# Kernel tuning notes

Measured on AMD Instinct MI355X. Metric: run time of the kernel, lower is better.

The kernel has to match this reference:

```python
import jax, jax.numpy as jnp
import numpy as np

B = 1
H_IMG, W_IMG = 64, 64
NF = H_IMG * W_IMG          # 4096 front/query tokens
NS = 1024                   # satellite tokens (32x32 grid)
SAT_IN, FRONT_IN = 768, 320
NH, HD = 8, 64
MD = NH * HD                # 512
GHID, GHD = 128, 16
GMD = NH * GHD              # 128
GEO_RATIO, ROPE_BASE = 0.5, 10000.0
LAMBDA_GEO, LAMBDA_GEOM = 1.0, 1.0
EPS = 1e-5


def _linear(x, w, b):
    return x @ w.T + b


def _layernorm(x, g, b):
    m = x.mean(-1, keepdims=True)
    v = jnp.var(x, axis=-1, keepdims=True)
    return (x - m) / jnp.sqrt(v + EPS) * g + b


def _georope(t, xy):
    """Continuous 2D (x,y) rotary embedding on the first GEO_RATIO fraction of head_dim.
    t: [B,NH,N,HD], xy: [B,N,2]."""
    rot = int(HD * GEO_RATIO)       # rotated dims (32)
    axis = rot // 2                 # dims per spatial axis (16)
    half = axis // 2                # frequency pairs per axis (8)
    inv_freq = ROPE_BASE ** (-jnp.arange(half, dtype=t.dtype) / half)

    def rot_axis(a, coord):
        th = coord[:, None, :, None] * inv_freq   # [B,1,N,half]
        c, s = jnp.cos(th), jnp.sin(th)
        a1, a2 = a[..., :half], a[..., half:]
        return jnp.concatenate([a1 * c - a2 * s, a1 * s + a2 * c], axis=-1)

    tx = rot_axis(t[..., :axis], xy[..., 0])
    ty = rot_axis(t[..., axis:rot], xy[..., 1])
    return jnp.concatenate([tx, ty, t[..., rot:]], axis=-1)


def _heads(x, hd):
    b, n, _ = x.shape
    return x.reshape(b, n, NH, hd).transpose(0, 2, 1, 3)


def setup_inputs() -> dict:
    key = jax.random.key(0)
    ks = iter(jax.random.split(key, 64))

    def w(*shape):
        return jax.random.normal(next(ks), shape, jnp.float32) / np.sqrt(shape[-1]).astype(np.float32)

    z = lambda n: jnp.zeros((n,), jnp.float32)
    o = lambda n: jnp.ones((n,), jnp.float32)
    return {
        "front_feat": jax.random.normal(next(ks), (B, FRONT_IN, H_IMG, W_IMG), jnp.float32),
        "front_bev_xy": jax.random.uniform(next(ks), (B, NF, 2), jnp.float32, -1.0, 1.0),
        "sat_tokens": jax.random.normal(next(ks), (B, NS, SAT_IN), jnp.float32),
        "sat_xy": jax.random.uniform(next(ks), (B, NS, 2), jnp.float32, -1.0, 1.0),
        "front_plucker": jax.random.normal(next(ks), (B, NF, 6), jnp.float32),
        "pos_w1": w(MD, 2), "pos_b1": z(MD), "pos_w2": w(MD, MD), "pos_b2": z(MD),
        "fa_w": w(MD, FRONT_IN), "fa_b": z(MD), "fa_ln_g": o(MD), "fa_ln_b": z(MD),
        "qn_g": o(MD), "qn_b": z(MD),
        "sa_w": w(MD, SAT_IN), "sa_b": z(MD), "sa_ln_g": o(MD), "sa_ln_b": z(MD),
        "wq": w(MD, MD), "bq": z(MD), "wk": w(MD, MD), "bk": z(MD), "wv": w(MD, MD), "bv": z(MD),
        "plk_w1": w(GHID, 6), "plk_b1": z(GHID), "plk_w2": w(GHID, GHID), "plk_b2": z(GHID),
        "sxy_w1": w(GHID, 2), "sxy_b1": z(GHID), "sxy_w2": w(GHID, GHID), "sxy_b2": z(GHID),
        "gqn_g": o(GHID), "gqn_b": z(GHID), "gkn_g": o(GHID), "gkn_b": z(GHID),
        "wqg": w(GMD, GHID), "bqg": z(GMD), "wkg": w(GMD, GHID), "bkg": z(GMD),
    }


def reference(front_feat, front_bev_xy, sat_tokens, sat_xy, front_plucker,
              pos_w1, pos_b1, pos_w2, pos_b2, fa_w, fa_b, fa_ln_g, fa_ln_b,
              qn_g, qn_b, sa_w, sa_b, sa_ln_g, sa_ln_b, wq, bq, wk, bk, wv, bv,
              plk_w1, plk_b1, plk_w2, plk_b2, sxy_w1, sxy_b1, sxy_w2, sxy_b2,
              gqn_g, gqn_b, gkn_g, gkn_b, wqg, bqg, wkg, bkg):
    b = front_feat.shape[0]
    ff = front_feat.reshape(b, FRONT_IN, NF).transpose(0, 2, 1)      # [B,NF,C]
    pos = _linear(jax.nn.silu(_linear(front_bev_xy, pos_w1, pos_b1)), pos_w2, pos_b2)
    feat = _layernorm(_linear(ff, fa_w, fa_b), fa_ln_g, fa_ln_b)
    q_embed = _layernorm(pos + feat, qn_g, qn_b)
    sat_feat = _layernorm(_linear(sat_tokens, sa_w, sa_b), sa_ln_g, sa_ln_b)
    q = _heads(_linear(q_embed, wq, bq), HD)                         # [B,H,NF,HD]
    k = _heads(_linear(sat_feat, wk, bk), HD)                        # [B,H,NS,HD]
    v = _heads(_linear(sat_feat, wv, bv), HD)
    qr = _georope(q, front_bev_xy)
    kr = _georope(k, sat_xy)
    logits = jnp.einsum('bhqd,bhkd->bhqk', qr, kr) / np.float32(np.sqrt(HD))
    # learned geometric Q/K stream (Plucker rays vs sat xy)
    plk = _layernorm(_linear(jax.nn.silu(_linear(front_plucker, plk_w1, plk_b1)), plk_w2, plk_b2), gqn_g, gqn_b)
    sgf = _layernorm(_linear(jax.nn.silu(_linear(sat_xy, sxy_w1, sxy_b1)), sxy_w2, sxy_b2), gkn_g, gkn_b)
    qg = _heads(_linear(plk, wqg, bqg), GHD)
    kg = _heads(_linear(sgf, wkg, bkg), GHD)
    logits = logits + LAMBDA_GEOM * (jnp.einsum('bhqd,bhkd->bhqk', qg, kg) / np.float32(np.sqrt(GHD)))
    # additive pairwise squared-distance bias, broadcast over heads
    dist2 = ((front_bev_xy[:, :, None, :] - sat_xy[:, None, :, :]) ** 2).sum(-1)   # [B,NF,NS]
    logits = logits - LAMBDA_GEO * dist2[:, None]
    attn = jax.nn.softmax(logits, axis=-1)
    read = jnp.einsum('bhqk,bhkd->bhqd', attn, v)
    return read.transpose(0, 2, 1, 3).reshape(b, NF, MD)
```

## Files before the change

kernel.cpp:

```cpp
#include <hip/hip_runtime.h>
#include <hip/hip_bf16.h>
#include <stdint.h>

#define NF 4096
#define NS 1024
#define MD 512
#define HD 64
#define DA 96
#define GHID 128

#define L2E 1.44269504f
#define S2L 1.6986436f
#define SMAX 12.0f

typedef unsigned short u16;
typedef __attribute__((ext_vector_type(8))) short bf8v;
typedef __attribute__((ext_vector_type(4))) float f4v;

__device__ __forceinline__ u16 f2bf(float f) {
  __hip_bfloat16 h = __float2bfloat16(f);
  return __builtin_bit_cast(u16, h);
}
__device__ __forceinline__ float bf2f(u16 u) {
  union { unsigned u; float f; } v; v.u = ((unsigned)u) << 16; return v.f;
}
__device__ __forceinline__ f4v mfma16(bf8v a, bf8v b, f4v c) {
  return __builtin_amdgcn_mfma_f32_16x16x32_bf16(a, b, c, 0, 0, 0);
}
__device__ __forceinline__ void gld16(const void* g, void* l) {
  __builtin_amdgcn_global_load_lds(
      (const __attribute__((address_space(1))) unsigned int*)g,
      (__attribute__((address_space(3))) unsigned int*)l, 16, 0, 0);
}

#define OFF_POSW2 0
#define OFF_FAW   262144
#define OFF_SAW   425984
#define OFF_WQ    819200
#define OFF_WKV   1081344
#define OFF_PLKW2 1605632
#define OFF_SXYW2 1622016
#define OFF_WQG   1638400
#define OFF_WKG   1654784
#define OFF_SATT  1671168
#define TOTW      2457600

#define EPI_OUT  0
#define EPI_ROPE 1
#define EPI_VT   2
#define EPI_GEO  3

__global__ __launch_bounds__(256) void k_l0(
    const float* __restrict__ s0, const float* __restrict__ s1,
    const float* __restrict__ s2, const float* __restrict__ s3,
    const float* __restrict__ s4, const float* __restrict__ s5,
    const float* __restrict__ s6, const float* __restrict__ s7,
    const float* __restrict__ s8, const float* __restrict__ s9,
    const float* __restrict__ s10, u16* __restrict__ pool,
    const float* __restrict__ bk, const float* __restrict__ bv,
    float* __restrict__ bkv,
    const float* __restrict__ ff, u16* __restrict__ ffT,
    const float* __restrict__ in0, const float* __restrict__ w0,
    const float* __restrict__ b0, u16* __restrict__ o0,
    const float* __restrict__ in1, const float* __restrict__ w1,
    const float* __restrict__ b1, u16* __restrict__ o1,
    const float* __restrict__ in2, const float* __restrict__ w2,
    const float* __restrict__ b2, u16* __restrict__ o2,
    u16* __restrict__ Qaug, u16* __restrict__ Kaug, float* __restrict__ kk2) {
  __shared__ u16 sT[32][72];
  int blk = blockIdx.x, t = threadIdx.x;
  if (blk < 2401) {
    int i4 = blk * 256 + t;
    if (i4 < TOTW / 4) {
      int idx = i4 * 4;
      const float* src; int off;
      if      (idx < OFF_FAW)   { src = s0;  off = OFF_POSW2; }
      else if (idx < OFF_SAW)   { src = s1;  off = OFF_FAW; }
      else if (idx < OFF_WQ)    { src = s2;  off = OFF_SAW; }
      else if (idx < OFF_WKV)   { src = s3;  off = OFF_WQ; }
      else if (idx < 1343488)   { src = s4;  off = OFF_WKV; }
      else if (idx < OFF_PLKW2) { src = s5;  off = 1343488; }
      else if (idx < OFF_SXYW2) { src = s6;  off = OFF_PLKW2; }
      else if (idx < OFF_WQG)   { src = s7;  off = OFF_SXYW2; }
      else if (idx < OFF_WKG)   { src = s8;  off = OFF_WQG; }
      else if (idx < OFF_SATT)  { src = s9;  off = OFF_WKG; }
      else                      { src = s10; off = OFF_SATT; }
      float4 v = *(const float4*)(src + (idx - off));
      ushort4 o;
      o.x = f2bf(v.x); o.y = f2bf(v.y); o.z = f2bf(v.z); o.w = f2bf(v.w);
      *(ushort4*)(pool + idx) = o;
    } else if (i4 < TOTW / 4 + 256) {
      int j = (i4 - TOTW / 4) * 4;
#pragma unroll
      for (int e = 0; e < 4; ++e) {
        int b = j + e;
        bkv[b] = (b < 512) ? bk[b] : bv[b - 512];
      }
    }
  } else if (blk < 3041) {
    int lb = blk - 2401;
    int n0 = (lb & 63) * 64, c0 = (lb >> 6) * 32;
    {
      int cr = t >> 3, nc = (t & 7) * 8;
      const float* src = ff + (size_t)(c0 + cr) * NF + n0 + nc;
      float4 v0 = *(const float4*)src, v1 = *(const float4*)(src + 4);
      bf8v p;
      p[0]=(short)f2bf(v0.x); p[1]=(short)f2bf(v0.y); p[2]=(short)f2bf(v0.z); p[3]=(short)f2bf(v0.w);
      p[4]=(short)f2bf(v1.x); p[5]=(short)f2bf(v1.y); p[6]=(short)f2bf(v1.z); p[7]=(short)f2bf(v1.w);
      *(bf8v*)&sT[cr][nc] = p;
    }
    __syncthreads();
    {
      int r = t >> 2, cc = (t & 3) * 8;
      bf8v p;
#pragma unroll
      for (int e = 0; e < 8; ++e) p[e] = (short)sT[cc + e][r];
      *(bf8v*)(ffT + (size_t)(n0 + r) * 320 + c0 + cc) = p;
    }
  } else if (blk < 13793) {
    int lb = blk - 3041;
    const float *in, *w, *b; u16* o; int mlog, K, idx;
    if (lb < 8192)       { in = in0; w = w0; b = b0; o = o0; mlog = 9; K = 2; idx = lb * 256 + t; }
    else if (lb < 10240) { in = in1; w = w1; b = b1; o = o1; mlog = 7; K = 6; idx = (lb - 8192) * 256 + t; }
    else                 { in = in2; w = w2; b = b2; o = o2; mlog = 7; K = 2; idx = (lb - 10240) * 256 + t; }
    int M = 1 << mlog;
    int n = idx >> mlog, m = idx & (M - 1);
    float acc = b[m];
    for (int k = 0; k < K; ++k) acc += in[n * K + k] * w[m * K + k];
    o[idx] = f2bf(acc / (1.f + __expf(-acc)));
  } else {
    int id = (blk - 13793) * 256 + t;
    int side = id >= NF * 8;
    int lid = side ? id - NF * 8 : id;
    int n = lid >> 3, h = lid & 7;
    const float* xy = side ? in2 : in0;
    u16* aug = side ? Kaug : Qaug;
    int nrows = side ? NS : NF;
    float x = xy[n * 2], y = xy[n * 2 + 1];
    bf8v p0, z;
#pragma unroll
    for (int e = 0; e < 8; ++e) { p0[e] = 0; z[e] = 0; }
    p0[0] = (short)f2bf(S2L * x);
    p0[1] = (short)f2bf(S2L * y);
    u16* dst = aug + ((size_t)h * nrows + n) * DA + 80;
    *(bf8v*)dst = p0;
    *(bf8v*)(dst + 8) = z;
    if (side && h == 0) kk2[n] = L2E * (x * x + y * y) + SMAX;
  }
}

__device__ __forceinline__ void gemm_body(const u16* __restrict__ A, const u16* __restrict__ W,
                                          const float* __restrict__ bias, u16* __restrict__ out,
                                          int m0, int n0, int N, int K,
                                          int mode, float scale, const float* __restrict__ xy,
                                          u16* __restrict__ aug, int nrows) {
  constexpr int MR = 2, NR = 2;
  __shared__ u16 sA[2][64 * 64];
  __shared__ u16 sB[2][64 * 64];
  const int tid = threadIdx.x, w = tid >> 6, lane = tid & 63;
  const int l16 = lane & 15, lh = lane >> 4;
  const int wr = w >> 1, wc = w & 1;

  f4v acc[MR][NR];
#pragma unroll
  for (int m = 0; m < MR; ++m)
#pragma unroll
    for (int j = 0; j < NR; ++j) acc[m][j] = (f4v){0.f, 0.f, 0.f, 0.f};

  auto stageA = [&](int buf, int k0) {
#pragma unroll
    for (int i = 0; i < 2; ++i) {
      int c = i * 256 + tid;
      int row = c >> 3, cp = c & 7;
      int sc_ = cp ^ (row & 7);
      gld16(A + (size_t)(m0 + row) * K + k0 + sc_ * 8, &sA[buf][c * 8]);
    }
  };
  auto stageB = [&](int buf, int k0) {
#pragma unroll
    for (int i = 0; i < 2; ++i) {
      int c = i * 256 + tid;
      int row = c >> 3, cp = c & 7;
      int sc_ = cp ^ (row & 7);
      gld16(W + (size_t)(n0 + row) * K + k0 + sc_ * 8, &sB[buf][c * 8]);
    }
  };

  stageA(0, 0); stageB(0, 0);
  __syncthreads();
  const int NK = K >> 6;
  for (int ks = 0; ks < NK; ++ks) {
    int nb = ks & 1;
    if (ks + 1 < NK) { stageA(nb ^ 1, (ks + 1) * 64); stageB(nb ^ 1, (ks + 1) * 64); }
#pragma unroll
    for (int kk = 0; kk < 2; ++kk) {
      bf8v af[MR], bfr[NR];
#pragma unroll
      for (int m = 0; m < MR; ++m) {
        int row = wr * 32 + m * 16 + l16;
        int cp = (kk * 4 + lh) ^ (row & 7);
        af[m] = *(const bf8v*)&sA[nb][row * 64 + cp * 8];
      }
#pragma unroll
      for (int j = 0; j < NR; ++j) {
        int row = wc * 32 + j * 16 + l16;
        int cp = (kk * 4 + lh) ^ (row & 7);
        bfr[j] = *(const bf8v*)&sB[nb][row * 64 + cp * 8];
      }
#pragma unroll
      for (int m = 0; m < MR; ++m)
#pragma unroll
        for (int j = 0; j < NR; ++j) acc[m][j] = mfma16(af[m], bfr[j], acc[m][j]);
    }
    __syncthreads();
  }

  if (mode == EPI_OUT) {
#pragma unroll
    for (int m = 0; m < MR; ++m) {
      int grow = m0 + wr * 32 + m * 16 + (lh << 2);
#pragma unroll
      for (int j = 0; j < NR; ++j) {
        int gcol = n0 + wc * 32 + j * 16 + l16;
        float bvs = bias ? bias[gcol] : 0.f;
#pragma unroll
        for (int r = 0; r < 4; ++r)
          out[(size_t)(grow + r) * N + gcol] = f2bf(acc[m][j][r] + bvs);
      }
    }
  } else if (mode == EPI_ROPE) {
    float fr = __expf(-(float)(l16 & 7) * 1.1512925465f);
#pragma unroll
    for (int m = 0; m < MR; ++m) {
      int grow = m0 + wr * 32 + m * 16 + (lh << 2);
#pragma unroll
      for (int j = 0; j < NR; ++j) {
        int gcol = n0 + wc * 32 + j * 16 + l16;
        int h = gcol >> 6, d = gcol & 63;
        float bvs = bias[gcol];
#pragma unroll
        for (int r = 0; r < 4; ++r) {
          int n = grow + r;
          float val = acc[m][j][r] + bvs;
          float part = __shfl_xor(val, 8);
          float outv = val;
          if (wc == 0) {
            float2 c2 = ((const float2*)xy)[n];
            float coord = j ? c2.y : c2.x;
            float sn, cs;
            __sincosf(coord * fr, &sn, &cs);
            outv = (l16 & 8) ? (part * sn + val * cs) : (val * cs - part * sn);
          }
          aug[((size_t)h * nrows + n) * DA + d] = f2bf(outv * scale);
        }
      }
    }
  } else if (mode == EPI_VT) {
#pragma unroll
    for (int m = 0; m < MR; ++m) {
      int grow = m0 + wr * 32 + m * 16 + (lh << 2);
#pragma unroll
      for (int j = 0; j < NR; ++j) {
        int gcol = n0 + wc * 32 + j * 16 + l16;
        int vcol = gcol - 512;
        int h = vcol >> 6, d = vcol & 63;
        float bvs = bias[gcol];
        ushort4 o;
        o.x = f2bf(acc[m][j][0] + bvs);
        o.y = f2bf(acc[m][j][1] + bvs);
        o.z = f2bf(acc[m][j][2] + bvs);
        o.w = f2bf(acc[m][j][3] + bvs);
        *(ushort4*)(aug + ((size_t)(h * 64 + d)) * NS + grow) = o;
      }
    }
  } else {
#pragma unroll
    for (int m = 0; m < MR; ++m) {
      int grow = m0 + wr * 32 + m * 16 + (lh << 2);
#pragma unroll
      for (int j = 0; j < NR; ++j) {
        int gcol = n0 + wc * 32 + j * 16 + l16;
        int h = gcol >> 4, dg = gcol & 15;
        float bvs = bias[gcol];
#pragma unroll
        for (int r = 0; r < 4; ++r)
          aug[((size_t)h * nrows + grow + r) * DA + 64 + dg] = f2bf((acc[m][j][r] + bvs) * scale);
      }
    }
  }
}

struct GP { const u16* A; const u16* W; const float* bias; u16* out;
            int K; int N; int M; int mode; float scale; const float* xy;
            u16* aug; int nrows; };

__device__ __forceinline__ void gemm_dispatch(const GP& g, int blk) {
  int mt = g.M >> 6;
  int m0 = (blk % mt) * 64, n0 = (blk / mt) * 64;
  gemm_body(g.A, g.W, g.bias, g.out, m0, n0, g.N, g.K,
            g.mode, g.scale, g.xy, g.aug, g.nrows);
}

__global__ __launch_bounds__(256) void k_gemm_L1(GP a, GP b, GP c, GP d, GP e) {
  int blk = blockIdx.x;
  if (blk < 512)       gemm_dispatch(a, blk);
  else if (blk < 1024) gemm_dispatch(b, blk - 512);
  else if (blk < 1152) gemm_dispatch(c, blk - 1024);
  else if (blk < 1280) gemm_dispatch(d, blk - 1152);
  else                 gemm_dispatch(e, blk - 1280);
}
__global__ __launch_bounds__(256) void k_gemm_L2(GP a, GP b, GP c, GP d, u16* VTp) {
  int blk = blockIdx.x;
  if (blk < 512) {
    gemm_dispatch(a, blk);
  } else if (blk < 768) {
    int lb = blk - 512;
    int m0 = (lb & 15) * 64, n0 = (lb >> 4) * 64;
    if (n0 >= 512)
      gemm_body(b.A, b.W, b.bias, b.out, m0, n0, b.N, b.K, EPI_VT, 1.f, nullptr, VTp, NS);
    else
      gemm_body(b.A, b.W, b.bias, b.out, m0, n0, b.N, b.K, b.mode, b.scale, b.xy, b.aug, b.nrows);
  } else if (blk < 896) {
    gemm_dispatch(c, blk - 768);
  } else {
    gemm_dispatch(d, blk - 896);
  }
}

__global__ __launch_bounds__(256) void k_ln_all(
    const u16* __restrict__ feat_pre, const u16* __restrict__ pos,
    const float* __restrict__ fg, const float* __restrict__ fb,
    const float* __restrict__ qg, const float* __restrict__ qb2,
    u16* __restrict__ q_embed,
    const u16* __restrict__ satf_pre, const float* __restrict__ sg,
    const float* __restrict__ sb, u16* __restrict__ satf,
    const u16* __restrict__ ginq, const u16* __restrict__ gink,
    const float* __restrict__ ggq, const float* __restrict__ gbq,
    const float* __restrict__ ggk, const float* __restrict__ gbk,
    u16* __restrict__ goutq, u16* __restrict__ goutk) {
  int blk = blockIdx.x;
  int w = threadIdx.x >> 6, lane = threadIdx.x & 63;
  if (blk < 1024) {
    int row = blk * 4 + w;
    bf8v v = *(const bf8v*)(feat_pre + (size_t)row * 512 + lane * 8);
    float x[8];
#pragma unroll
    for (int e = 0; e < 8; ++e) x[e] = bf2f((u16)v[e]);
    float s = 0.f, q = 0.f;
#pragma unroll
    for (int e = 0; e < 8; ++e) { s += x[e]; q += x[e] * x[e]; }
#pragma unroll
    for (int mm = 1; mm < 64; mm <<= 1) { s += __shfl_xor(s, mm); q += __shfl_xor(q, mm); }
    float mean = s / 512.f, var = q / 512.f - mean * mean;
    float rstd = rsqrtf(var + 1e-5f);
    bf8v vp = *(const bf8v*)(pos + (size_t)row * 512 + lane * 8);
#pragma unroll
    for (int e = 0; e < 8; ++e)
      x[e] = (x[e] - mean) * rstd * fg[lane * 8 + e] + fb[lane * 8 + e] + bf2f((u16)vp[e]);
    s = 0.f; q = 0.f;
#pragma unroll
    for (int e = 0; e < 8; ++e) { s += x[e]; q += x[e] * x[e]; }
#pragma unroll
    for (int mm = 1; mm < 64; mm <<= 1) { s += __shfl_xor(s, mm); q += __shfl_xor(q, mm); }
    mean = s / 512.f; var = q / 512.f - mean * mean;
    rstd = rsqrtf(var + 1e-5f);
    bf8v ov;
#pragma unroll
    for (int e = 0; e < 8; ++e)
      ov[e] = (short)f2bf((x[e] - mean) * rstd * qg[lane * 8 + e] + qb2[lane * 8 + e]);
    *(bf8v*)(q_embed + (size_t)row * 512 + lane * 8) = ov;
  } else if (blk < 1280) {
    int row = (blk - 1024) * 4 + w;
    bf8v v = *(const bf8v*)(satf_pre + (size_t)row * 512 + lane * 8);
    float x[8];
#pragma unroll
    for (int e = 0; e < 8; ++e) x[e] = bf2f((u16)v[e]);
    float s = 0.f, q = 0.f;
#pragma unroll
    for (int e = 0; e < 8; ++e) { s += x[e]; q += x[e] * x[e]; }
#pragma unroll
    for (int mm = 1; mm < 64; mm <<= 1) { s += __shfl_xor(s, mm); q += __shfl_xor(q, mm); }
    float mean = s / 512.f, var = q / 512.f - mean * mean;
    float rstd = rsqrtf(var + 1e-5f);
    bf8v ov;
#pragma unroll
    for (int e = 0; e < 8; ++e)
      ov[e] = (short)f2bf((x[e] - mean) * rstd * sg[lane * 8 + e] + sb[lane * 8 + e]);
    *(bf8v*)(satf + (size_t)row * 512 + lane * 8) = ov;
  } else {
    int row = (blk - 1280) * 4 + w;
    const u16* in; const float *g, *b; u16* out;
    if (row < 4096) { in = ginq; g = ggq; b = gbq; out = goutq; }
    else { row -= 4096; in = gink; g = ggk; b = gbk; out = goutk; }
    uint32_t v = *(const uint32_t*)(in + (size_t)row * 128 + lane * 2);
    float x0 = bf2f((u16)(v & 0xffff)), x1 = bf2f((u16)(v >> 16));
    float s = x0 + x1, q = x0 * x0 + x1 * x1;
#pragma unroll
    for (int mm = 1; mm < 64; mm <<= 1) { s += __shfl_xor(s, mm); q += __shfl_xor(q, mm); }
    float mean = s / 128.f, var = q / 128.f - mean * mean;
    float rstd = rsqrtf(var + 1e-5f);
    u16 o0 = f2bf((x0 - mean) * rstd * g[lane * 2] + b[lane * 2]);
    u16 o1 = f2bf((x1 - mean) * rstd * g[lane * 2 + 1] + b[lane * 2 + 1]);
    *(uint32_t*)(out + (size_t)row * 128 + lane * 2) = (uint32_t)o0 | ((uint32_t)o1 << 16);
  }
}

__global__ __launch_bounds__(256, 4) void k_flash(const u16* __restrict__ Qa,
                                                  const u16* __restrict__ Ka,
                                                  const u16* __restrict__ VT,
                                                  const float* __restrict__ kk2,
                                                  u16* __restrict__ Opart,
                                                  float* __restrict__ lbuf) {
  const int h = blockIdx.y, qb = blockIdx.x, sp = blockIdx.z;
  const int tid = threadIdx.x, w = tid >> 6, lane = tid & 63;
  const int l16 = lane & 15, lh = lane >> 4;
  __shared__ u16 sK[64][104];
  __shared__ u16 sV[64][72];
  __shared__ u16 sP[4][16][72];
  __shared__ float sKK[512];

  ((float2*)sKK)[tid] = ((const float2*)(kk2 + sp * 512))[tid];

  const int qrow = qb * 64 + w * 16 + l16;
  bf8v qf[3];
#pragma unroll
  for (int c = 0; c < 3; ++c)
    qf[c] = *(const bf8v*)(Qa + (size_t)(h * NF + qrow) * DA + c * 32 + lh * 8);

  bf8v ONES;
#pragma unroll
  for (int i = 0; i < 8; ++i) ONES[i] = (short)0x3F80;

  const int crow = qb * 64 + w * 16 + (lh << 2);
  float l_run[4] = {0.f, 0.f, 0.f, 0.f};
  f4v accO[4];
#pragma unroll
  for (int d = 0; d < 4; ++d) accO[d] = (f4v){0.f, 0.f, 0.f, 0.f};

  const int kt0 = sp * 8;
  bf8v kreg[3], vreg[2];
  auto sload = [&](int t8) {
    int kb = (kt0 + t8) * 64;
#pragma unroll
    for (int i = 0; i < 3; ++i) {
      int c = tid + i * 256; int r = c / 12, off = (c % 12) * 8;
      kreg[i] = *(const bf8v*)(Ka + ((size_t)(h * NS) + kb + r) * DA + off);
    }
#pragma unroll
    for (int i = 0; i < 2; ++i) {
      int c = tid + i * 256; int d = c >> 3, off = (c & 7) * 8;
      vreg[i] = *(const bf8v*)(VT + ((size_t)(h * HD) + d) * NS + kb + off);
    }
  };
  auto swrite = [&]() {
#pragma unroll
    for (int i = 0; i < 3; ++i) {
      int c = tid + i * 256; int r = c / 12, off = (c % 12) * 8;
      *(bf8v*)&sK[r][off] = kreg[i];
    }
#pragma unroll
    for (int i = 0; i < 2; ++i) {
      int c = tid + i * 256; int d = c >> 3, off = (c & 7) * 8;
      *(bf8v*)&sV[d][off] = vreg[i];
    }
  };

  sload(0); swrite();
  __syncthreads();
  for (int t8 = 0; t8 < 8; ++t8) {
    if (t8 < 7) sload(t8 + 1);
#pragma unroll
    for (int j = 0; j < 4; ++j) {
      f4v s4 = (f4v){0.f, 0.f, 0.f, 0.f};
#pragma unroll
      for (int c = 0; c < 3; ++c) {
        bf8v kf = *(const bf8v*)&sK[j * 16 + l16][c * 32 + lh * 8];
        s4 = mfma16(qf[c], kf, s4);
      }
      float ck = sKK[t8 * 64 + j * 16 + l16];
#pragma unroll
      for (int r = 0; r < 4; ++r) {
        float pv = exp2f(s4[r] - ck);
        sP[w][(lh << 2) + r][j * 16 + l16] = f2bf(pv);
      }
    }
    bf8v pf0 = *(const bf8v*)&sP[w][l16][lh * 8];
    bf8v pf1 = *(const bf8v*)&sP[w][l16][32 + lh * 8];
    f4v ls = (f4v){0.f, 0.f, 0.f, 0.f};
    ls = mfma16(pf0, ONES, ls);
    ls = mfma16(pf1, ONES, ls);
#pragma unroll
    for (int r = 0; r < 4; ++r) l_run[r] += ls[r];
#pragma unroll
    for (int c = 0; c < 2; ++c) {
      bf8v pf = (c == 0) ? pf0 : pf1;
#pragma unroll
      for (int d = 0; d < 4; ++d) {
        bf8v vf = *(const bf8v*)&sV[d * 16 + l16][c * 32 + lh * 8];
        accO[d] = mfma16(pf, vf, accO[d]);
      }
    }
    __syncthreads();
    if (t8 < 7) swrite();
    __syncthreads();
  }
  size_t obase = (size_t)(sp * 8 + h) * NF + crow;
#pragma unroll
  for (int d = 0; d < 4; ++d)
#pragma unroll
    for (int r = 0; r < 4; ++r)
      Opart[(obase + r) * 64 + d * 16 + l16] = f2bf(accO[d][r]);
  if (l16 == 0) {
#pragma unroll
    for (int r = 0; r < 4; ++r) lbuf[obase + r] = l_run[r];
  }
}

__global__ void k_combine(const u16* __restrict__ Opart, const float* __restrict__ lbuf,
                          float* __restrict__ out) {
  int i4 = blockIdx.x * 256 + threadIdx.x;
  int n = i4 >> 7;
  int c4 = i4 & 127, h = c4 >> 4, d4 = c4 & 15;
  float l = lbuf[(size_t)h * NF + n] + lbuf[(size_t)(8 + h) * NF + n];
  float rl = 1.f / l;
  ushort4 a = ((const ushort4*)(Opart + ((size_t)h * NF + n) * 64))[d4];
  ushort4 b = ((const ushort4*)(Opart + ((size_t)(8 + h) * NF + n) * 64))[d4];
  float4 r;
  r.x = (bf2f(a.x) + bf2f(b.x)) * rl;
  r.y = (bf2f(a.y) + bf2f(b.y)) * rl;
  r.z = (bf2f(a.z) + bf2f(b.z)) * rl;
  r.w = (bf2f(a.w) + bf2f(b.w)) * rl;
  ((float4*)out)[i4] = r;
}

extern "C" void kernel_launch(void* const* d_in, const int* in_sizes, int n_in,
                              void* d_out, int out_size, void* d_ws, size_t ws_size,
                              hipStream_t stream) {
  (void)in_sizes; (void)n_in; (void)out_size; (void)ws_size;
  const float* front_feat = (const float*)d_in[0];
  const float* bev_xy     = (const float*)d_in[1];
  const float* sat_tokens = (const float*)d_in[2];
  const float* sat_xy     = (const float*)d_in[3];
  const float* plucker    = (const float*)d_in[4];
  const float* pos_w1 = (const float*)d_in[5];
  const float* pos_b1 = (const float*)d_in[6];
  const float* pos_w2 = (const float*)d_in[7];
  const float* pos_b2 = (const float*)d_in[8];
  const float* fa_w   = (const float*)d_in[9];
  const float* fa_b   = (const float*)d_in[10];
  const float* fa_ln_g = (const float*)d_in[11];
  const float* fa_ln_b = (const float*)d_in[12];
  const float* qn_g   = (const float*)d_in[13];
  const float* qn_b   = (const float*)d_in[14];
  const float* sa_w   = (const float*)d_in[15];
  const float* sa_b   = (const float*)d_in[16];
  const float* sa_ln_g = (const float*)d_in[17];
  const float* sa_ln_b = (const float*)d_in[18];
  const float* wq = (const float*)d_in[19];
  const float* bq = (const float*)d_in[20];
  const float* wk = (const float*)d_in[21];
  const float* bk = (const float*)d_in[22];
  const float* wv = (const float*)d_in[23];
  const float* bv = (const float*)d_in[24];
  const float* plk_w1 = (const float*)d_in[25];
  const float* plk_b1 = (const float*)d_in[26];
  const float* plk_w2 = (const float*)d_in[27];
  const float* plk_b2 = (const float*)d_in[28];
  const float* sxy_w1 = (const float*)d_in[29];
  const float* sxy_b1 = (const float*)d_in[30];
  const float* sxy_w2 = (const float*)d_in[31];
  const float* sxy_b2 = (const float*)d_in[32];
  const float* gqn_g = (const float*)d_in[33];
  const float* gqn_b = (const float*)d_in[34];
  const float* gkn_g = (const float*)d_in[35];
  const float* gkn_b = (const float*)d_in[36];
  const float* wqg = (const float*)d_in[37];
  const float* bqg = (const float*)d_in[38];
  const float* wkg = (const float*)d_in[39];
  const float* bkg = (const float*)d_in[40];

  char* ws = (char*)d_ws;
  size_t off = 0;
  auto alloc = [&](size_t bytes) {
    size_t r = off;
    off += (bytes + 255) & ~(size_t)255;
    return r;
  };
  u16*   wpool   = (u16*)(ws + alloc((size_t)TOTW * 2));
  float* bkv     = (float*)(ws + alloc(1024 * 4));
  u16*   ffT     = (u16*)(ws + alloc((size_t)NF * 320 * 2));
  u16*   pos_h   = (u16*)(ws + alloc((size_t)NF * MD * 2));
  u16*   plk_h   = (u16*)(ws + alloc((size_t)NF * GHID * 2));
  u16*   sxy_h   = (u16*)(ws + alloc((size_t)NS * GHID * 2));
  u16*   pos     = (u16*)(ws + alloc((size_t)NF * MD * 2));
  u16*   feat_pre= (u16*)(ws + alloc((size_t)NF * MD * 2));
  u16*   satf_pre= (u16*)(ws + alloc((size_t)NS * MD * 2));
  u16*   satf    = (u16*)(ws + alloc((size_t)NS * MD * 2));
  u16*   q_embed = (u16*)(ws + alloc((size_t)NF * MD * 2));
  u16*   plk2    = (u16*)(ws + alloc((size_t)NF * GHID * 2));
  u16*   sxy2    = (u16*)(ws + alloc((size_t)NS * GHID * 2));
  u16*   Qaug    = (u16*)(ws + alloc((size_t)8 * NF * DA * 2));
  u16*   Kaug    = (u16*)(ws + alloc((size_t)8 * NS * DA * 2));
  u16*   VT      = (u16*)(ws + alloc((size_t)8 * HD * NS * 2));
  float* kk2     = (float*)(ws + alloc((size_t)NS * 4));
  u16*   Opart   = (u16*)(ws + alloc((size_t)2 * 8 * NF * 64 * 2));
  float* lbuf    = (float*)(ws + alloc((size_t)2 * 8 * NF * 4));
  u16* plk_ln = plk_h;
  u16* sgf    = sxy_h;

  dim3 b256(256);
  k_l0<<<dim3(13953), b256, 0, stream>>>(
      pos_w2, fa_w, sa_w, wq, wk, wv, plk_w2, sxy_w2, wqg, wkg, sat_tokens,
      wpool, bk, bv, bkv, front_feat, ffT,
      bev_xy, pos_w1, pos_b1, pos_h,
      plucker, plk_w1, plk_b1, plk_h,
      sat_xy, sxy_w1, sxy_b1, sxy_h,
      Qaug, Kaug, kk2);

  GP gpos {pos_h, wpool + OFF_POSW2, pos_b2, pos, 512, 512, 4096, EPI_OUT, 0.f, nullptr, nullptr, 0};
  GP gfeat{ffT, wpool + OFF_FAW, fa_b, feat_pre, 320, 512, 4096, EPI_OUT, 0.f, nullptr, nullptr, 0};
  GP gsat {wpool + OFF_SATT, wpool + OFF_SAW, sa_b, satf_pre, 768, 512, 1024, EPI_OUT, 0.f, nullptr, nullptr, 0};
  GP ggq1 {plk_h, wpool + OFF_PLKW2, plk_b2, plk2, 128, 128, 4096, EPI_OUT, 0.f, nullptr, nullptr, 0};
  GP ggk1 {sxy_h, wpool + OFF_SXYW2, sxy_b2, sxy2, 128, 128, 1024, EPI_OUT, 0.f, nullptr, nullptr, 0};
  k_gemm_L1<<<dim3(1312), b256, 0, stream>>>(gpos, gfeat, gsat, ggq1, ggk1);

  k_ln_all<<<dim3(2560), b256, 0, stream>>>(
      feat_pre, pos, fa_ln_g, fa_ln_b, qn_g, qn_b, q_embed,
      satf_pre, sa_ln_g, sa_ln_b, satf,
      plk2, sxy2, gqn_g, gqn_b, gkn_g, gkn_b, plk_ln, sgf);

  GP gq  {q_embed, wpool + OFF_WQ, bq, nullptr, 512, 512, 4096, EPI_ROPE, 0.125f * L2E, bev_xy, Qaug, NF};
  GP gkv {satf, wpool + OFF_WKV, bkv, nullptr, 512, 1024, 1024, EPI_ROPE, 1.f, sat_xy, Kaug, NS};
  GP ggq2{plk_ln, wpool + OFF_WQG, bqg, nullptr, 128, 128, 4096, EPI_GEO, 0.25f * L2E, nullptr, Qaug, NF};
  GP ggk2{sgf, wpool + OFF_WKG, bkg, nullptr, 128, 128, 1024, EPI_GEO, 1.f, nullptr, Kaug, NS};
  k_gemm_L2<<<dim3(928), b256, 0, stream>>>(gq, gkv, ggq2, ggk2, VT);

  k_flash<<<dim3(NF / 64, 8, 2), b256, 0, stream>>>(Qaug, Kaug, VT, kk2, Opart, lbuf);
  k_combine<<<dim3(NF * MD / 4 / 256), b256, 0, stream>>>(Opart, lbuf, (float*)d_out);
}
```

Measured before the change: 79.76 us.

## Use 128x64 GEMM tiles for first-layer projections and shrink flash LDS padding

Adds a 128x64 tile GEMM body in which each wave computes a 32x64 slab, and uses it for all five first-layer GEMMs. This halves the block count and raises operand reuse per loaded tile. Separately, the flash kernel's shared-memory row padding is reduced and the occupancy hint goes from 4 to 5 blocks. The smaller padding may bring back LDS bank conflicts, and fewer GEMM blocks may underfill the GPU on the smaller problems.

```diff
diff --git a/kernel.cpp b/kernel.cpp
--- a/kernel.cpp
+++ b/kernel.cpp
@@ -149,6 +149,81 @@
   }
 }
 
+__device__ __forceinline__ void gemm_body128(const u16* __restrict__ A, const u16* __restrict__ W,
+                                             const float* __restrict__ bias, u16* __restrict__ out,
+                                             int m0, int n0, int N, int K) {
+  __shared__ u16 sA[2][128 * 64];
+  __shared__ u16 sB[2][64 * 64];
+  const int tid = threadIdx.x, w = tid >> 6, lane = tid & 63;
+  const int l16 = lane & 15, lh = lane >> 4;
+
+  f4v acc[2][4];
+#pragma unroll
+  for (int m = 0; m < 2; ++m)
+#pragma unroll
+    for (int j = 0; j < 4; ++j) acc[m][j] = (f4v){0.f, 0.f, 0.f, 0.f};
+
+  auto stageA = [&](int buf, int k0) {
+#pragma unroll
+    for (int i = 0; i < 4; ++i) {
+      int c = i * 256 + tid;
+      int row = c >> 3, cp = c & 7;
+      int sc_ = cp ^ (row & 7);
+      gld16(A + (size_t)(m0 + row) * K + k0 + sc_ * 8, &sA[buf][c * 8]);
+    }
+  };
+  auto stageB = [&](int buf, int k0) {
+#pragma unroll
+    for (int i = 0; i < 2; ++i) {
+      int c = i * 256 + tid;
+      int row = c >> 3, cp = c & 7;
+      int sc_ = cp ^ (row & 7);
+      gld16(W + (size_t)(n0 + row) * K + k0 + sc_ * 8, &sB[buf][c * 8]);
+    }
+  };
+
+  stageA(0, 0); stageB(0, 0);
+  __syncthreads();
+  const int NK = K >> 6;
+  for (int ks = 0; ks < NK; ++ks) {
+    int nb = ks & 1;
+    if (ks + 1 < NK) { stageA(nb ^ 1, (ks + 1) * 64); stageB(nb ^ 1, (ks + 1) * 64); }
+#pragma unroll
+    for (int kk = 0; kk < 2; ++kk) {
+      bf8v af[2], bfr[4];
+#pragma unroll
+      for (int m = 0; m < 2; ++m) {
+        int row = w * 32 + m * 16 + l16;
+        int cp = (kk * 4 + lh) ^ (row & 7);
+        af[m] = *(const bf8v*)&sA[nb][row * 64 + cp * 8];
+      }
+#pragma unroll
+      for (int j = 0; j < 4; ++j) {
+        int row = j * 16 + l16;
+        int cp = (kk * 4 + lh) ^ (row & 7);
+        bfr[j] = *(const bf8v*)&sB[nb][row * 64 + cp * 8];
+      }
+#pragma unroll
+      for (int m = 0; m < 2; ++m)
+#pragma unroll
+        for (int j = 0; j < 4; ++j) acc[m][j] = mfma16(af[m], bfr[j], acc[m][j]);
+    }
+    __syncthreads();
+  }
+#pragma unroll
+  for (int m = 0; m < 2; ++m) {
+    int grow = m0 + w * 32 + m * 16 + (lh << 2);
+#pragma unroll
+    for (int j = 0; j < 4; ++j) {
+      int gcol = n0 + j * 16 + l16;
+      float bvs = bias ? bias[gcol] : 0.f;
+#pragma unroll
+      for (int r = 0; r < 4; ++r)
+        out[(size_t)(grow + r) * N + gcol] = f2bf(acc[m][j][r] + bvs);
+    }
+  }
+}
+
 __device__ __forceinline__ void gemm_body(const u16* __restrict__ A, const u16* __restrict__ W,
                                           const float* __restrict__ bias, u16* __restrict__ out,
                                           int m0, int n0, int N, int K,
@@ -294,6 +369,11 @@
             int K; int N; int M; int mode; float scale; const float* xy;
             u16* aug; int nrows; };
 
+__device__ __forceinline__ void gemm_dispatch128(const GP& g, int blk) {
+  int mt = g.M >> 7;
+  int m0 = (blk % mt) * 128, n0 = (blk / mt) * 64;
+  gemm_body128(g.A, g.W, g.bias, g.out, m0, n0, g.N, g.K);
+}
 __device__ __forceinline__ void gemm_dispatch(const GP& g, int blk) {
   int mt = g.M >> 6;
   int m0 = (blk % mt) * 64, n0 = (blk / mt) * 64;
@@ -303,11 +383,11 @@
 
 __global__ __launch_bounds__(256) void k_gemm_L1(GP a, GP b, GP c, GP d, GP e) {
   int blk = blockIdx.x;
-  if (blk < 512)       gemm_dispatch(a, blk);
-  else if (blk < 1024) gemm_dispatch(b, blk - 512);
-  else if (blk < 1152) gemm_dispatch(c, blk - 1024);
-  else if (blk < 1280) gemm_dispatch(d, blk - 1152);
-  else                 gemm_dispatch(e, blk - 1280);
+  if (blk < 256)       gemm_dispatch128(a, blk);
+  else if (blk < 512)  gemm_dispatch128(b, blk - 256);
+  else if (blk < 576)  gemm_dispatch128(c, blk - 512);
+  else if (blk < 640)  gemm_dispatch128(d, blk - 576);
+  else                 gemm_dispatch128(e, blk - 640);
 }
 __global__ __launch_bounds__(256) void k_gemm_L2(GP a, GP b, GP c, GP d, u16* VTp) {
   int blk = blockIdx.x;
@@ -405,7 +485,7 @@
   }
 }
 
-__global__ __launch_bounds__(256, 4) void k_flash(const u16* __restrict__ Qa,
+__global__ __launch_bounds__(256, 5) void k_flash(const u16* __restrict__ Qa,
                                                   const u16* __restrict__ Ka,
                                                   const u16* __restrict__ VT,
                                                   const float* __restrict__ kk2,
@@ -414,9 +494,9 @@
   const int h = blockIdx.y, qb = blockIdx.x, sp = blockIdx.z;
   const int tid = threadIdx.x, w = tid >> 6, lane = tid & 63;
   const int l16 = lane & 15, lh = lane >> 4;
-  __shared__ u16 sK[64][104];
-  __shared__ u16 sV[64][72];
-  __shared__ u16 sP[4][16][72];
+  __shared__ u16 sK[64][100];
+  __shared__ u16 sV[64][68];
+  __shared__ u16 sP[4][16][68];
   __shared__ float sKK[512];
 
   ((float2*)sKK)[tid] = ((const float2*)(kk2 + sp * 512))[tid];
@@ -622,7 +702,7 @@
   GP gsat {wpool + OFF_SATT, wpool + OFF_SAW, sa_b, satf_pre, 768, 512, 1024, EPI_OUT, 0.f, nullptr, nullptr, 0};
   GP ggq1 {plk_h, wpool + OFF_PLKW2, plk_b2, plk2, 128, 128, 4096, EPI_OUT, 0.f, nullptr, nullptr, 0};
   GP ggk1 {sxy_h, wpool + OFF_SXYW2, sxy_b2, sxy2, 128, 128, 1024, EPI_OUT, 0.f, nullptr, nullptr, 0};
-  k_gemm_L1<<<dim3(1312), b256, 0, stream>>>(gpos, gfeat, gsat, ggq1, ggk1);
+  k_gemm_L1<<<dim3(656), b256, 0, stream>>>(gpos, gfeat, gsat, ggq1, ggk1);
 
   k_ln_all<<<dim3(2560), b256, 0, stream>>>(
       feat_pre, pos, fa_ln_g, fa_ln_b, qn_g, qn_b, q_embed,
```

After: 79.25 us. No clear change (-0.6%).
